# Kernel tuning notes

Hardware: AMD Instinct MI355X
Metric: run time of the kernel (lower is better)

The kernel has to match this reference:

```python
import jax, jax.numpy as jnp
import numpy as np
from math import sqrt

D_MODEL = 512
HEADS = 8
D_K = D_MODEL // HEADS
DIM_FFN = 2048
EPS = 1e-6


def setup_inputs() -> dict:
    key = jax.random.key(0)
    ks = jax.random.split(key, 16)
    b, s = 2, 256
    inp = {
        "x": jax.random.normal(ks[0], (b, s, D_MODEL), dtype=jnp.float32),
        "connection_bias_k": jax.random.normal(ks[1], (b, s, s, D_MODEL), dtype=jnp.float32) * 0.02,
        "connection_bias_v": jax.random.normal(ks[2], (b, s, s, D_MODEL), dtype=jnp.float32) * 0.02,
        "mask": jnp.zeros((b, s), dtype=jnp.int32),
        "Wq": jax.random.normal(ks[3], (D_MODEL, D_MODEL), dtype=jnp.float32) / sqrt(D_MODEL),
        "bq": jnp.zeros((D_MODEL,), dtype=jnp.float32),
        "Wk": jax.random.normal(ks[4], (D_MODEL, D_MODEL), dtype=jnp.float32) / sqrt(D_MODEL),
        "bk": jnp.zeros((D_MODEL,), dtype=jnp.float32),
        "Wv": jax.random.normal(ks[5], (D_MODEL, D_MODEL), dtype=jnp.float32) / sqrt(D_MODEL),
        "bv": jnp.zeros((D_MODEL,), dtype=jnp.float32),
        "Wo": jax.random.normal(ks[6], (D_MODEL, D_MODEL), dtype=jnp.float32) / sqrt(D_MODEL),
        "bo": jnp.zeros((D_MODEL,), dtype=jnp.float32),
        "alpha1": jnp.ones((D_MODEL,), dtype=jnp.float32),
        "beta1": jnp.zeros((D_MODEL,), dtype=jnp.float32),
        "alpha2": jnp.ones((D_MODEL,), dtype=jnp.float32),
        "beta2": jnp.zeros((D_MODEL,), dtype=jnp.float32),
        "W1": jax.random.normal(ks[7], (DIM_FFN, D_MODEL), dtype=jnp.float32) / sqrt(D_MODEL),
        "b1": jnp.zeros((DIM_FFN,), dtype=jnp.float32),
        "W2": jax.random.normal(ks[8], (D_MODEL, DIM_FFN), dtype=jnp.float32) / sqrt(DIM_FFN),
        "b2": jnp.zeros((D_MODEL,), dtype=jnp.float32),
    }
    return inp


def _norm(x, alpha, beta):
    # torch .std() is unbiased (ddof=1); note std is added to eps OUTSIDE variance
    mu = jnp.mean(x, axis=-1, keepdims=True)
    sd = jnp.std(x, axis=-1, ddof=1, keepdims=True)
    return alpha * (x - mu) / (sd + EPS) + beta


def reference(x, connection_bias_k, connection_bias_v, mask,
              Wq, bq, Wk, bk, Wv, bv, Wo, bo,
              alpha1, beta1, alpha2, beta2, W1, b1, W2, b2):
    b, s, _ = x.shape
    h, dk = HEADS, D_K

    x2 = _norm(x, alpha1, beta1)
    # projections -> [b, h, s, dk]
    q = (x2 @ Wq.T + bq).reshape(b, s, h, dk).transpose(0, 2, 1, 3)
    k = (x2 @ Wk.T + bk).reshape(b, s, h, dk).transpose(0, 2, 1, 3)
    v = (x2 @ Wv.T + bv).reshape(b, s, h, dk).transpose(0, 2, 1, 3)

    # biases reshaped to (b, s1, s2, h, dk); biased_k[b,h,i,j] = k[b,h,j] + bias[b,j,i,h]
    bk_r = connection_bias_k.reshape(b, s, s, h, dk)
    bv_r = connection_bias_v.reshape(b, s, s, h, dk)

    # scores[b,h,i,j] = q_i . (k_j + bias_k[b,j,i,h]) / sqrt(dk)
    scores = (jnp.einsum('bhid,bhjd->bhij', q, k)
              + jnp.einsum('bhid,bjihd->bhij', q, bk_r)) / sqrt(dk)

    # mask [b,s] -> [b,1,s,1], broadcast over heads and key dim (matches torch)
    m = mask[:, None, :, None]
    scores = jnp.where(m == 1, -1e9, scores)
    attn = jax.nn.softmax(scores, axis=-1)

    # out[b,h,i,d] = sum_j attn[b,h,i,j] * (v[b,h,j] + bias_v[b,j,i,h])
    out = (jnp.einsum('bhij,bhjd->bhid', attn, v)
           + jnp.einsum('bhij,bjihd->bhid', attn, bv_r))
    concat = out.transpose(0, 2, 1, 3).reshape(b, s, D_MODEL)
    attn_out = concat @ Wo.T + bo

    x = x + attn_out
    x2 = _norm(x, alpha2, beta2)
    ff = jax.nn.relu(x2 @ W1.T + b1) @ W2.T + b2
    return x + ff
```

## Files before the change

kernel.cpp:

```cpp
#include <hip/hip_runtime.h>
#include <math.h>

#define D_MODEL 512
#define NHEADS 8
#define DK 64
#define DFFN 2048

typedef __attribute__((ext_vector_type(8))) __bf16 bf16x8;
typedef __attribute__((ext_vector_type(4))) float floatx4;

__global__ __launch_bounds__(256) void ln_kernel(
    const float* __restrict__ x, const float* __restrict__ alpha,
    const float* __restrict__ beta, __bf16* __restrict__ y) {
  int row = blockIdx.x;
  int t = threadIdx.x;
  const float* xr = x + (size_t)row * D_MODEL;
  float2 v = ((const float2*)xr)[t];
  __shared__ float rs[256], rq[256];
  rs[t] = v.x + v.y;
  rq[t] = v.x * v.x + v.y * v.y;
  __syncthreads();
  for (int o = 128; o > 0; o >>= 1) {
    if (t < o) { rs[t] += rs[t + o]; rq[t] += rq[t + o]; }
    __syncthreads();
  }
  float mu = rs[0] * (1.0f / D_MODEL);
  float var = (rq[0] - (float)D_MODEL * mu * mu) * (1.0f / (D_MODEL - 1));
  float inv = 1.0f / (sqrtf(fmaxf(var, 0.0f)) + 1e-6f);
  float2 a2 = ((const float2*)alpha)[t];
  float2 b2 = ((const float2*)beta)[t];
  union { __bf16 h2[2]; unsigned int u; } pk;
  pk.h2[0] = (__bf16)(a2.x * (v.x - mu) * inv + b2.x);
  pk.h2[1] = (__bf16)(a2.y * (v.y - mu) * inv + b2.y);
  *(unsigned int*)(y + (size_t)row * D_MODEL + 2 * t) = pk.u;
}

struct Seg { const float* src; __bf16* dst; int n4; };
struct Segs6 { Seg s[6]; };
__global__ __launch_bounds__(256) void cast6(Segs6 cs) {
  Seg sg = cs.s[blockIdx.y];
  int stride = gridDim.x * 256;
  for (int idx = blockIdx.x * 256 + threadIdx.x; idx < sg.n4; idx += stride) {
    float4 f = ((const float4*)sg.src)[idx];
    union { __bf16 h[4]; uint2 u; } pk;
    pk.h[0] = (__bf16)f.x; pk.h[1] = (__bf16)f.y;
    pk.h[2] = (__bf16)f.z; pk.h[3] = (__bf16)f.w;
    ((uint2*)sg.dst)[idx] = pk.u;
  }
}

__global__ __launch_bounds__(256) void pack_bias(
    const float* __restrict__ bq, const float* __restrict__ bk,
    const float* __restrict__ bv, float* __restrict__ dst) {
  int idx = blockIdx.x * 256 + threadIdx.x;
  if (idx >= 3 * D_MODEL) return;
  float v = idx < 512 ? bq[idx] : (idx < 1024 ? bk[idx - 512] : bv[idx - 1024]);
  dst[idx] = v;
}

template <int RELU, int OUT_BF16>
__global__ __launch_bounds__(64) void wave_gemm(
    const __bf16* __restrict__ A, int lda, const __bf16* __restrict__ B, int ldb,
    const float* __restrict__ bias, const float* __restrict__ res,
    void* __restrict__ Cv, int N, int K) {
  int lane = threadIdx.x;
  int r16 = lane & 15;
  int ko = (lane >> 4) * 8;
  int m0 = blockIdx.y * 32, n0 = blockIdx.x * 32;
  const __bf16* A0 = A + (size_t)(m0 + r16) * lda + ko;
  const __bf16* A1 = A0 + (size_t)16 * lda;
  const __bf16* B0 = B + (size_t)(n0 + r16) * ldb + ko;
  const __bf16* B1 = B0 + (size_t)16 * ldb;
  floatx4 acc00 = {0.f, 0.f, 0.f, 0.f};
  floatx4 acc01 = acc00, acc10 = acc00, acc11 = acc00;
#pragma unroll 4
  for (int k0 = 0; k0 < K; k0 += 32) {
    bf16x8 a0 = *(const bf16x8*)(A0 + k0);
    bf16x8 a1 = *(const bf16x8*)(A1 + k0);
    bf16x8 b0 = *(const bf16x8*)(B0 + k0);
    bf16x8 b1 = *(const bf16x8*)(B1 + k0);
    acc00 = __builtin_amdgcn_mfma_f32_16x16x32_bf16(a0, b0, acc00, 0, 0, 0);
    acc01 = __builtin_amdgcn_mfma_f32_16x16x32_bf16(a0, b1, acc01, 0, 0, 0);
    acc10 = __builtin_amdgcn_mfma_f32_16x16x32_bf16(a1, b0, acc10, 0, 0, 0);
    acc11 = __builtin_amdgcn_mfma_f32_16x16x32_bf16(a1, b1, acc11, 0, 0, 0);
  }
  int col = lane & 15, rb = (lane >> 4) * 4;
  floatx4 accs[2][2] = {{acc00, acc01}, {acc10, acc11}};
#pragma unroll
  for (int i = 0; i < 2; ++i) {
#pragma unroll
    for (int j = 0; j < 2; ++j) {
#pragma unroll
      for (int r = 0; r < 4; ++r) {
        int row = m0 + i * 16 + rb + r;
        int cc = n0 + j * 16 + col;
        float v = accs[i][j][r] + bias[cc];
        if (res) v += res[(size_t)row * N + cc];
        if (RELU) v = fmaxf(v, 0.0f);
        if (OUT_BF16)
          ((__bf16*)Cv)[(size_t)row * N + cc] = (__bf16)v;
        else
          ((float*)Cv)[(size_t)row * N + cc] = v;
      }
    }
  }
}

__global__ __launch_bounds__(256) void attn_kernel(
    const float* __restrict__ qkv, int ldq,
    const float* __restrict__ cbk, const float* __restrict__ cbv,
    const int* __restrict__ mask, __bf16* __restrict__ concat, int s) {
  int i = blockIdx.x % s;
  int b = blockIdx.x / s;
  int t = threadIdx.x;
  int w = t >> 6;
  int lane = t & 63;
  int h = lane >> 3;

  __shared__ float sc[NHEADS][257];
  __shared__ float sums[NHEADS];
  __shared__ float part[4][D_MODEL];

  size_t tok_i = (size_t)(b * s + i);
  const float* qp = qkv + tok_i * ldq + lane * 8;
  float4 q0 = *(const float4*)(qp);
  float4 q1 = *(const float4*)(qp + 4);

  for (int jj = 0; jj < 64; ++jj) {
    int j = w * 64 + jj;
    size_t tok_j = (size_t)(b * s + j);
    const float* kp = qkv + tok_j * ldq + 512 + lane * 8;
    const float* cp = cbk + (tok_j * s + i) * D_MODEL + lane * 8;
    float4 k0 = *(const float4*)(kp);
    float4 k1 = *(const float4*)(kp + 4);
    float4 c0 = *(const float4*)(cp);
    float4 c1 = *(const float4*)(cp + 4);
    float d = q0.x * (k0.x + c0.x) + q0.y * (k0.y + c0.y) +
              q0.z * (k0.z + c0.z) + q0.w * (k0.w + c0.w) +
              q1.x * (k1.x + c1.x) + q1.y * (k1.y + c1.y) +
              q1.z * (k1.z + c1.z) + q1.w * (k1.w + c1.w);
    d += __shfl_xor(d, 1);
    d += __shfl_xor(d, 2);
    d += __shfl_xor(d, 4);
    if ((lane & 7) == 0) sc[h][j] = d * 0.125f;
  }
  __syncthreads();

  {
    int hh = 2 * w + (lane >> 5);
    int l32 = lane & 31;
    bool masked = (mask[b * s + i] == 1);
    float vals[8];
    float mx = -1e30f;
#pragma unroll
    for (int kk = 0; kk < 8; ++kk) {
      float xv = sc[hh][l32 + kk * 32];
      if (masked) xv = -1e9f;
      vals[kk] = xv;
      mx = fmaxf(mx, xv);
    }
    for (int m = 1; m < 32; m <<= 1) mx = fmaxf(mx, __shfl_xor(mx, m, 32));
    float ls = 0.f;
#pragma unroll
    for (int kk = 0; kk < 8; ++kk) {
      float e = expf(vals[kk] - mx);
      sc[hh][l32 + kk * 32] = e;
      ls += e;
    }
    for (int m = 1; m < 32; m <<= 1) ls += __shfl_xor(ls, m, 32);
    if (l32 == 0) sums[hh] = ls;
  }
  __syncthreads();

  float4 a0 = {0.f, 0.f, 0.f, 0.f};
  float4 a1 = {0.f, 0.f, 0.f, 0.f};
  for (int jj = 0; jj < 64; ++jj) {
    int j = w * 64 + jj;
    size_t tok_j = (size_t)(b * s + j);
    const float* vp = qkv + tok_j * ldq + 1024 + lane * 8;
    const float* cp = cbv + (tok_j * s + i) * D_MODEL + lane * 8;
    float4 v0 = *(const float4*)(vp);
    float4 v1 = *(const float4*)(vp + 4);
    float4 c0 = *(const float4*)(cp);
    float4 c1 = *(const float4*)(cp + 4);
    float pj = sc[h][j];
    a0.x += pj * (v0.x + c0.x); a0.y += pj * (v0.y + c0.y);
    a0.z += pj * (v0.z + c0.z); a0.w += pj * (v0.w + c0.w);
    a1.x += pj * (v1.x + c1.x); a1.y += pj * (v1.y + c1.y);
    a1.z += pj * (v1.z + c1.z); a1.w += pj * (v1.w + c1.w);
  }
  *(float4*)&part[w][lane * 8] = a0;
  *(float4*)&part[w][lane * 8 + 4] = a1;
  __syncthreads();

  int d0 = t * 2;
  float inv = 1.0f / sums[d0 >> 6];
  float o0 = (part[0][d0] + part[1][d0] + part[2][d0] + part[3][d0]) * inv;
  float o1 = (part[0][d0 + 1] + part[1][d0 + 1] + part[2][d0 + 1] + part[3][d0 + 1]) * inv;
  union { __bf16 h2[2]; unsigned int u; } pk;
  pk.h2[0] = (__bf16)o0;
  pk.h2[1] = (__bf16)o1;
  *(unsigned int*)(concat + tok_i * D_MODEL + d0) = pk.u;
}

extern "C" void kernel_launch(void* const* d_in, const int* in_sizes, int n_in,
                              void* d_out, int out_size, void* d_ws, size_t ws_size,
                              hipStream_t stream) {
  const float* x      = (const float*)d_in[0];
  const float* cbk    = (const float*)d_in[1];
  const float* cbv    = (const float*)d_in[2];
  const int*   mask   = (const int*)d_in[3];
  const float* Wq     = (const float*)d_in[4];
  const float* bq     = (const float*)d_in[5];
  const float* Wk     = (const float*)d_in[6];
  const float* bk     = (const float*)d_in[7];
  const float* Wv     = (const float*)d_in[8];
  const float* bv     = (const float*)d_in[9];
  const float* Wo     = (const float*)d_in[10];
  const float* bo     = (const float*)d_in[11];
  const float* alpha1 = (const float*)d_in[12];
  const float* beta1  = (const float*)d_in[13];
  const float* alpha2 = (const float*)d_in[14];
  const float* beta2  = (const float*)d_in[15];
  const float* W1     = (const float*)d_in[16];
  const float* b1     = (const float*)d_in[17];
  const float* W2     = (const float*)d_in[18];
  const float* b2     = (const float*)d_in[19];

  int bs = in_sizes[0] / D_MODEL;
  int s  = in_sizes[1] / in_sizes[0];

  char* wp = (char*)d_ws;
  auto carve = [&](size_t bytes) {
    char* p = wp;
    wp += (bytes + 255) & ~(size_t)255;
    return p;
  };
  __bf16* x2    = (__bf16*)carve((size_t)bs * D_MODEL * 2);
  __bf16* wqkv  = (__bf16*)carve((size_t)3 * D_MODEL * D_MODEL * 2);
  __bf16* wo_b  = (__bf16*)carve((size_t)D_MODEL * D_MODEL * 2);
  __bf16* w1_b  = (__bf16*)carve((size_t)DFFN * D_MODEL * 2);
  __bf16* w2_b  = (__bf16*)carve((size_t)D_MODEL * DFFN * 2);
  float*  bqkv  = (float*)carve((size_t)3 * D_MODEL * 4);
  float*  qkv   = (float*)carve((size_t)bs * 3 * D_MODEL * 4);
  __bf16* conc  = (__bf16*)carve((size_t)bs * D_MODEL * 2);
  float*  xres  = (float*)carve((size_t)bs * D_MODEL * 4);
  __bf16* x2b   = (__bf16*)carve((size_t)bs * D_MODEL * 2);
  __bf16* f1    = (__bf16*)carve((size_t)bs * DFFN * 2);

  Segs6 cs;
  cs.s[0] = {Wq, wqkv,                 D_MODEL * D_MODEL / 4};
  cs.s[1] = {Wk, wqkv + D_MODEL * D_MODEL,     D_MODEL * D_MODEL / 4};
  cs.s[2] = {Wv, wqkv + 2 * D_MODEL * D_MODEL, D_MODEL * D_MODEL / 4};
  cs.s[3] = {Wo, wo_b, D_MODEL * D_MODEL / 4};
  cs.s[4] = {W1, w1_b, DFFN * D_MODEL / 4};
  cs.s[5] = {W2, w2_b, D_MODEL * DFFN / 4};
  cast6<<<dim3(256, 6), 256, 0, stream>>>(cs);
  pack_bias<<<6, 256, 0, stream>>>(bq, bk, bv, bqkv);

  ln_kernel<<<bs, 256, 0, stream>>>(x, alpha1, beta1, x2);

  wave_gemm<0, 0><<<dim3(3 * D_MODEL / 32, bs / 32), 64, 0, stream>>>(
      x2, D_MODEL, wqkv, D_MODEL, bqkv, nullptr, qkv, 3 * D_MODEL, D_MODEL);

  attn_kernel<<<bs, 256, 0, stream>>>(qkv, 3 * D_MODEL, cbk, cbv, mask, conc, s);

  wave_gemm<0, 0><<<dim3(D_MODEL / 32, bs / 32), 64, 0, stream>>>(
      conc, D_MODEL, wo_b, D_MODEL, bo, x, xres, D_MODEL, D_MODEL);

  ln_kernel<<<bs, 256, 0, stream>>>(xres, alpha2, beta2, x2b);

  wave_gemm<1, 1><<<dim3(DFFN / 32, bs / 32), 64, 0, stream>>>(
      x2b, D_MODEL, w1_b, D_MODEL, b1, nullptr, f1, DFFN, D_MODEL);

  wave_gemm<0, 0><<<dim3(D_MODEL / 32, bs / 32), 64, 0, stream>>>(
      f1, DFFN, w2_b, DFFN, b2, xres, d_out, D_MODEL, DFFN);
}
```

Measured before the change: 618.0 us.

## Widen attention blocks, use nontemporal bias loads, warp-per-row LayerNorm, fuse bias pack

The attention kernel now runs 512 threads (8 waves) per query row, each wave covering 32 keys. The large connection-bias streams are read with nontemporal loads and partially unrolled so more bytes are in flight. Softmax now maps one wave per head, and the output reduction sums 8 partials. LayerNorm is rewritten to use one wave per row with shuffle reductions and 16-byte loads and stores, and the QKV bias packing is folded into the weight-cast kernel to save a launch; the larger attention block may lower occupancy per CU.

Result: no change. 621.6 us (+0.6%).

```diff
diff --git a/kernel.cpp b/kernel.cpp
--- a/kernel.cpp
+++ b/kernel.cpp
@@ -8,36 +8,55 @@
 
 typedef __attribute__((ext_vector_type(8))) __bf16 bf16x8;
 typedef __attribute__((ext_vector_type(4))) float floatx4;
+typedef __attribute__((ext_vector_type(4))) float fvec4;
 
 __global__ __launch_bounds__(256) void ln_kernel(
     const float* __restrict__ x, const float* __restrict__ alpha,
     const float* __restrict__ beta, __bf16* __restrict__ y) {
-  int row = blockIdx.x;
-  int t = threadIdx.x;
-  const float* xr = x + (size_t)row * D_MODEL;
-  float2 v = ((const float2*)xr)[t];
-  __shared__ float rs[256], rq[256];
-  rs[t] = v.x + v.y;
-  rq[t] = v.x * v.x + v.y * v.y;
-  __syncthreads();
-  for (int o = 128; o > 0; o >>= 1) {
-    if (t < o) { rs[t] += rs[t + o]; rq[t] += rq[t + o]; }
-    __syncthreads();
-  }
-  float mu = rs[0] * (1.0f / D_MODEL);
-  float var = (rq[0] - (float)D_MODEL * mu * mu) * (1.0f / (D_MODEL - 1));
+  int w = threadIdx.x >> 6, lane = threadIdx.x & 63;
+  int row = blockIdx.x * 4 + w;
+  const float* xr = x + (size_t)row * D_MODEL + lane * 8;
+  fvec4 v0 = *(const fvec4*)xr;
+  fvec4 v1 = *(const fvec4*)(xr + 4);
+  float sm = v0.x + v0.y + v0.z + v0.w + v1.x + v1.y + v1.z + v1.w;
+  float qd = v0.x * v0.x + v0.y * v0.y + v0.z * v0.z + v0.w * v0.w +
+             v1.x * v1.x + v1.y * v1.y + v1.z * v1.z + v1.w * v1.w;
+  for (int m = 1; m < 64; m <<= 1) {
+    sm += __shfl_xor(sm, m);
+    qd += __shfl_xor(qd, m);
+  }
+  float mu = sm * (1.0f / D_MODEL);
+  float var = (qd - (float)D_MODEL * mu * mu) * (1.0f / (D_MODEL - 1));
   float inv = 1.0f / (sqrtf(fmaxf(var, 0.0f)) + 1e-6f);
-  float2 a2 = ((const float2*)alpha)[t];
-  float2 b2 = ((const float2*)beta)[t];
-  union { __bf16 h2[2]; unsigned int u; } pk;
-  pk.h2[0] = (__bf16)(a2.x * (v.x - mu) * inv + b2.x);
-  pk.h2[1] = (__bf16)(a2.y * (v.y - mu) * inv + b2.y);
-  *(unsigned int*)(y + (size_t)row * D_MODEL + 2 * t) = pk.u;
+  fvec4 a0 = *(const fvec4*)(alpha + lane * 8);
+  fvec4 a1 = *(const fvec4*)(alpha + lane * 8 + 4);
+  fvec4 b0 = *(const fvec4*)(beta + lane * 8);
+  fvec4 b1 = *(const fvec4*)(beta + lane * 8 + 4);
+  union { __bf16 h[8]; uint4 u4; } pk;
+  pk.h[0] = (__bf16)(a0.x * (v0.x - mu) * inv + b0.x);
+  pk.h[1] = (__bf16)(a0.y * (v0.y - mu) * inv + b0.y);
+  pk.h[2] = (__bf16)(a0.z * (v0.z - mu) * inv + b0.z);
+  pk.h[3] = (__bf16)(a0.w * (v0.w - mu) * inv + b0.w);
+  pk.h[4] = (__bf16)(a1.x * (v1.x - mu) * inv + b1.x);
+  pk.h[5] = (__bf16)(a1.y * (v1.y - mu) * inv + b1.y);
+  pk.h[6] = (__bf16)(a1.z * (v1.z - mu) * inv + b1.z);
+  pk.h[7] = (__bf16)(a1.w * (v1.w - mu) * inv + b1.w);
+  *(uint4*)(y + (size_t)row * D_MODEL + lane * 8) = pk.u4;
 }
 
 struct Seg { const float* src; __bf16* dst; int n4; };
 struct Segs6 { Seg s[6]; };
-__global__ __launch_bounds__(256) void cast6(Segs6 cs) {
+__global__ __launch_bounds__(256) void cast7(Segs6 cs,
+    const float* __restrict__ bq, const float* __restrict__ bk,
+    const float* __restrict__ bv, float* __restrict__ bqkv) {
+  if (blockIdx.y == 6) {
+    int idx = blockIdx.x * 256 + threadIdx.x;
+    if (idx < 3 * D_MODEL) {
+      float v = idx < 512 ? bq[idx] : (idx < 1024 ? bk[idx - 512] : bv[idx - 1024]);
+      bqkv[idx] = v;
+    }
+    return;
+  }
   Seg sg = cs.s[blockIdx.y];
   int stride = gridDim.x * 256;
   for (int idx = blockIdx.x * 256 + threadIdx.x; idx < sg.n4; idx += stride) {
@@ -47,15 +66,6 @@
     pk.h[2] = (__bf16)f.z; pk.h[3] = (__bf16)f.w;
     ((uint2*)sg.dst)[idx] = pk.u;
   }
-}
-
-__global__ __launch_bounds__(256) void pack_bias(
-    const float* __restrict__ bq, const float* __restrict__ bk,
-    const float* __restrict__ bv, float* __restrict__ dst) {
-  int idx = blockIdx.x * 256 + threadIdx.x;
-  if (idx >= 3 * D_MODEL) return;
-  float v = idx < 512 ? bq[idx] : (idx < 1024 ? bk[idx - 512] : bv[idx - 1024]);
-  dst[idx] = v;
 }
 
 template <int RELU, int OUT_BF16>
@@ -106,7 +116,7 @@
   }
 }
 
-__global__ __launch_bounds__(256) void attn_kernel(
+__global__ __launch_bounds__(512) void attn_kernel(
     const float* __restrict__ qkv, int ldq,
     const float* __restrict__ cbk, const float* __restrict__ cbv,
     const int* __restrict__ mask, __bf16* __restrict__ concat, int s) {
@@ -119,22 +129,25 @@
 
   __shared__ float sc[NHEADS][257];
   __shared__ float sums[NHEADS];
-  __shared__ float part[4][D_MODEL];
+  __shared__ float part[8][D_MODEL];
 
   size_t tok_i = (size_t)(b * s + i);
   const float* qp = qkv + tok_i * ldq + lane * 8;
-  float4 q0 = *(const float4*)(qp);
-  float4 q1 = *(const float4*)(qp + 4);
-
-  for (int jj = 0; jj < 64; ++jj) {
-    int j = w * 64 + jj;
-    size_t tok_j = (size_t)(b * s + j);
-    const float* kp = qkv + tok_j * ldq + 512 + lane * 8;
-    const float* cp = cbk + (tok_j * s + i) * D_MODEL + lane * 8;
-    float4 k0 = *(const float4*)(kp);
-    float4 k1 = *(const float4*)(kp + 4);
-    float4 c0 = *(const float4*)(cp);
-    float4 c1 = *(const float4*)(cp + 4);
+  fvec4 q0 = *(const fvec4*)(qp);
+  fvec4 q1 = *(const fvec4*)(qp + 4);
+
+  const float* kb  = qkv + (size_t)(b * s) * ldq + 512 + lane * 8;
+  const float* cbb = cbk + ((size_t)b * s * s + i) * (size_t)D_MODEL + lane * 8;
+
+#pragma unroll 4
+  for (int jj = 0; jj < 32; ++jj) {
+    int j = w * 32 + jj;
+    const float* kp = kb + (size_t)j * ldq;
+    const float* cp = cbb + (size_t)j * s * D_MODEL;
+    fvec4 k0 = *(const fvec4*)(kp);
+    fvec4 k1 = *(const fvec4*)(kp + 4);
+    fvec4 c0 = __builtin_nontemporal_load((const fvec4*)cp);
+    fvec4 c1 = __builtin_nontemporal_load(((const fvec4*)cp) + 1);
     float d = q0.x * (k0.x + c0.x) + q0.y * (k0.y + c0.y) +
               q0.z * (k0.z + c0.z) + q0.w * (k0.w + c0.w) +
               q1.x * (k1.x + c1.x) + q1.y * (k1.y + c1.y) +
@@ -147,60 +160,66 @@
   __syncthreads();
 
   {
-    int hh = 2 * w + (lane >> 5);
-    int l32 = lane & 31;
     bool masked = (mask[b * s + i] == 1);
-    float vals[8];
+    float vals[4];
     float mx = -1e30f;
 #pragma unroll
-    for (int kk = 0; kk < 8; ++kk) {
-      float xv = sc[hh][l32 + kk * 32];
+    for (int kk = 0; kk < 4; ++kk) {
+      float xv = sc[w][lane + kk * 64];
       if (masked) xv = -1e9f;
       vals[kk] = xv;
       mx = fmaxf(mx, xv);
     }
-    for (int m = 1; m < 32; m <<= 1) mx = fmaxf(mx, __shfl_xor(mx, m, 32));
+    for (int m = 1; m < 64; m <<= 1) mx = fmaxf(mx, __shfl_xor(mx, m));
     float ls = 0.f;
 #pragma unroll
-    for (int kk = 0; kk < 8; ++kk) {
+    for (int kk = 0; kk < 4; ++kk) {
       float e = expf(vals[kk] - mx);
-      sc[hh][l32 + kk * 32] = e;
+      sc[w][lane + kk * 64] = e;
       ls += e;
     }
-    for (int m = 1; m < 32; m <<= 1) ls += __shfl_xor(ls, m, 32);
-    if (l32 == 0) sums[hh] = ls;
+    for (int m = 1; m < 64; m <<= 1) ls += __shfl_xor(ls, m);
+    if (lane == 0) sums[w] = ls;
   }
   __syncthreads();
 
-  float4 a0 = {0.f, 0.f, 0.f, 0.f};
-  float4 a1 = {0.f, 0.f, 0.f, 0.f};
-  for (int jj = 0; jj < 64; ++jj) {
-    int j = w * 64 + jj;
-    size_t tok_j = (size_t)(b * s + j);
-    const float* vp = qkv + tok_j * ldq + 1024 + lane * 8;
-    const float* cp = cbv + (tok_j * s + i) * D_MODEL + lane * 8;
-    float4 v0 = *(const float4*)(vp);
-    float4 v1 = *(const float4*)(vp + 4);
-    float4 c0 = *(const float4*)(cp);
-    float4 c1 = *(const float4*)(cp + 4);
+  fvec4 a0 = {0.f, 0.f, 0.f, 0.f};
+  fvec4 a1 = {0.f, 0.f, 0.f, 0.f};
+  const float* vb  = qkv + (size_t)(b * s) * ldq + 1024 + lane * 8;
+  const float* cvb = cbv + ((size_t)b * s * s + i) * (size_t)D_MODEL + lane * 8;
+#pragma unroll 4
+  for (int jj = 0; jj < 32; ++jj) {
+    int j = w * 32 + jj;
+    const float* vp = vb + (size_t)j * ldq;
+    const float* cp = cvb + (size_t)j * s * D_MODEL;
+    fvec4 v0 = *(const fvec4*)(vp);
+    fvec4 v1 = *(const fvec4*)(vp + 4);
+    fvec4 c0 = __builtin_nontemporal_load((const fvec4*)cp);
+    fvec4 c1 = __builtin_nontemporal_load(((const fvec4*)cp) + 1);
     float pj = sc[h][j];
     a0.x += pj * (v0.x + c0.x); a0.y += pj * (v0.y + c0.y);
     a0.z += pj * (v0.z + c0.z); a0.w += pj * (v0.w + c0.w);
     a1.x += pj * (v1.x + c1.x); a1.y += pj * (v1.y + c1.y);
     a1.z += pj * (v1.z + c1.z); a1.w += pj * (v1.w + c1.w);
   }
-  *(float4*)&part[w][lane * 8] = a0;
-  *(float4*)&part[w][lane * 8 + 4] = a1;
+  *(fvec4*)&part[w][lane * 8] = a0;
+  *(fvec4*)&part[w][lane * 8 + 4] = a1;
   __syncthreads();
 
-  int d0 = t * 2;
-  float inv = 1.0f / sums[d0 >> 6];
-  float o0 = (part[0][d0] + part[1][d0] + part[2][d0] + part[3][d0]) * inv;
-  float o1 = (part[0][d0 + 1] + part[1][d0 + 1] + part[2][d0 + 1] + part[3][d0 + 1]) * inv;
-  union { __bf16 h2[2]; unsigned int u; } pk;
-  pk.h2[0] = (__bf16)o0;
-  pk.h2[1] = (__bf16)o1;
-  *(unsigned int*)(concat + tok_i * D_MODEL + d0) = pk.u;
+  if (t < 256) {
+    int d0 = t * 2;
+    float inv = 1.0f / sums[d0 >> 6];
+    float o0 = 0.f, o1 = 0.f;
+#pragma unroll
+    for (int ww = 0; ww < 8; ++ww) {
+      o0 += part[ww][d0];
+      o1 += part[ww][d0 + 1];
+    }
+    union { __bf16 h2[2]; unsigned int u; } pk;
+    pk.h2[0] = (__bf16)(o0 * inv);
+    pk.h2[1] = (__bf16)(o1 * inv);
+    *(unsigned int*)(concat + tok_i * D_MODEL + d0) = pk.u;
+  }
 }
 
 extern "C" void kernel_launch(void* const* d_in, const int* in_sizes, int n_in,
@@ -255,20 +274,19 @@
   cs.s[3] = {Wo, wo_b, D_MODEL * D_MODEL / 4};
   cs.s[4] = {W1, w1_b, DFFN * D_MODEL / 4};
   cs.s[5] = {W2, w2_b, D_MODEL * DFFN / 4};
-  cast6<<<dim3(256, 6), 256, 0, stream>>>(cs);
-  pack_bias<<<6, 256, 0, stream>>>(bq, bk, bv, bqkv);
-
-  ln_kernel<<<bs, 256, 0, stream>>>(x, alpha1, beta1, x2);
+  cast7<<<dim3(256, 7), 256, 0, stream>>>(cs, bq, bk, bv, bqkv);
+
+  ln_kernel<<<bs / 4, 256, 0, stream>>>(x, alpha1, beta1, x2);
 
   wave_gemm<0, 0><<<dim3(3 * D_MODEL / 32, bs / 32), 64, 0, stream>>>(
       x2, D_MODEL, wqkv, D_MODEL, bqkv, nullptr, qkv, 3 * D_MODEL, D_MODEL);
 
-  attn_kernel<<<bs, 256, 0, stream>>>(qkv, 3 * D_MODEL, cbk, cbv, mask, conc, s);
+  attn_kernel<<<bs, 512, 0, stream>>>(qkv, 3 * D_MODEL, cbk, cbv, mask, conc, s);
 
   wave_gemm<0, 0><<<dim3(D_MODEL / 32, bs / 32), 64, 0, stream>>>(
       conc, D_MODEL, wo_b, D_MODEL, bo, x, xres, D_MODEL, D_MODEL);
 
-  ln_kernel<<<bs, 256, 0, stream>>>(xres, alpha2, beta2, x2b);
+  ln_kernel<<<bs / 4, 256, 0, stream>>>(xres, alpha2, beta2, x2b);
 
   wave_gemm<1, 1><<<dim3(DFFN / 32, bs / 32), 64, 0, stream>>>(
       x2b, D_MODEL, w1_b, D_MODEL, b1, nullptr, f1, DFFN, D_MODEL);
```
